# Optimization experiments

Hardware: AMD Instinct MI355X
Metric: run time of the kernel (lower is better)

## Reference

```python
import jax, jax.numpy as jnp
import numpy as np

ROPE_BASE = 10000.0
NUM_HEADS = 16

def _rotate_half(x):
    d = x.shape[-1] // 2
    return jnp.concatenate([-x[..., d:], x[..., :d]], axis=-1)

def setup_inputs() -> dict:
    key = jax.random.key(0)
    ks = jax.random.split(key, 5)
    b, s, d = 1, 2048, 2048
    scale = 1.0 / np.sqrt(d)
    return {
        "hidden_states": jax.random.normal(ks[0], (b, s, d), jnp.float32),
        "wq": jax.random.normal(ks[1], (d, d), jnp.float32) * scale,
        "wk": jax.random.normal(ks[2], (d, d), jnp.float32) * scale,
        "wv": jax.random.normal(ks[3], (d, d), jnp.float32) * scale,
        "wo": jax.random.normal(ks[4], (d, d), jnp.float32) * scale,
        "position_ids": jnp.broadcast_to(jnp.arange(s, dtype=jnp.int32), (b, s)),
    }

def reference(hidden_states, wq, wk, wv, wo, position_ids):
    b, s, d = hidden_states.shape
    h = NUM_HEADS
    dh = d // h
    # q/k/v projections (torch Linear: y = x @ W^T), split heads -> bhsd
    def proj(w):
        return jnp.einsum('bsd,ed->bse', hidden_states, w).reshape(b, s, h, dh).transpose(0, 2, 1, 3)
    q, k, v = proj(wq), proj(wk), proj(wv)
    # rotary embedding (LLaMA style): freqs over half dim, duplicated
    inv_freq = 1.0 / (ROPE_BASE ** (jnp.arange(0, dh, 2, dtype=jnp.float32) / dh))
    t = jnp.arange(s, dtype=jnp.float32)
    freqs = jnp.einsum('s,f->sf', t, inv_freq)              # [s, dh/2]
    emb = jnp.concatenate([freqs, freqs], axis=-1)          # [s, dh]
    cos = jnp.cos(emb)[position_ids][:, None, :, :]         # [b,1,s,dh]
    sin = jnp.sin(emb)[position_ids][:, None, :, :]
    q = q * cos + _rotate_half(q) * sin
    k = k * cos + _rotate_half(k) * sin
    # full (non-causal) scaled dot-product attention, as in the SDPA fast path
    scores = jnp.einsum('bhqd,bhkd->bhqk', q, k) / jnp.sqrt(jnp.float32(dh))
    attn = jax.nn.softmax(scores, axis=-1)
    out = jnp.einsum('bhqk,bhkd->bhqd', attn, v)            # [b,h,s,dh]
    out = out.transpose(0, 2, 1, 3).reshape(b, s, d)
    return jnp.einsum('bsd,ed->bse', out, wo)
```

## Files before the change

kernel.cpp:

```cpp
#include <hip/hip_runtime.h>

typedef unsigned short ushort_t;
typedef unsigned int uint32;
typedef __attribute__((ext_vector_type(8))) short short8;
typedef __attribute__((ext_vector_type(4))) float f32x4;

#define LDS_LOAD16(gptr, lptr)                                                             \
  __builtin_amdgcn_global_load_lds((const __attribute__((address_space(1))) uint32*)(gptr),\
                                   (__attribute__((address_space(3))) uint32*)(lptr),      \
                                   16, 0, 0)

__device__ __forceinline__ ushort_t f2b(float f) {
  uint32 u = __builtin_bit_cast(uint32, f);
  u += 0x7fffu + ((u >> 16) & 1u);
  return (ushort_t)(u >> 16);
}
__device__ __forceinline__ float b2f(ushort_t b) {
  uint32 u = ((uint32)b) << 16;
  return __builtin_bit_cast(float, u);
}
__device__ __forceinline__ int swz4(int row) { return (row ^ (row >> 2)) & 3; }

constexpr size_t E = (size_t)2048 * 2048;

__global__ __launch_bounds__(256) void k_cvt5(const float* __restrict__ a0, const float* __restrict__ a1,
                                              const float* __restrict__ a2, const float* __restrict__ a3,
                                              const float* __restrict__ a4, ushort_t* __restrict__ out) {
  const float* srcs[5] = {a0, a1, a2, a3, a4};
  const float* s = srcs[blockIdx.y];
  size_t i = ((size_t)blockIdx.x * 256 + threadIdx.x) * 4;
  float4 v = *(const float4*)(s + i);
  ushort4 o;
  o.x = f2b(v.x); o.y = f2b(v.y); o.z = f2b(v.z); o.w = f2b(v.w);
  *(ushort4*)(out + (size_t)blockIdx.y * E + i) = o;
}

__global__ __launch_bounds__(256) void k_gemm_qkv(const ushort_t* __restrict__ A,
                                                  const ushort_t* __restrict__ B0,
                                                  const ushort_t* __restrict__ B1,
                                                  const ushort_t* __restrict__ B2,
                                                  ushort_t* __restrict__ Qm,
                                                  ushort_t* __restrict__ Km,
                                                  ushort_t* __restrict__ Vt) {
  __shared__ ushort_t As[128 * 32];
  __shared__ ushort_t Bs[128 * 32];
  const int tid = threadIdx.x;
  const int lane = tid & 63, wave = tid >> 6;
  const int quad = lane >> 4, l16 = lane & 15;
  const int wm = wave >> 1, wn = wave & 1;
  const int z = blockIdx.z;
  const ushort_t* Bp = (z == 0) ? B0 : (z == 1) ? B1 : B2;
  const size_t row0 = (size_t)blockIdx.y * 128, col0 = (size_t)blockIdx.x * 128;
  const int sw = swz4(l16);

  f32x4 zero = {0.f, 0.f, 0.f, 0.f};
  f32x4 acc[4][4];
#pragma unroll
  for (int i = 0; i < 4; ++i)
#pragma unroll
    for (int j = 0; j < 4; ++j) acc[i][j] = zero;

  for (int kt = 0; kt < 64; ++kt) {
#pragma unroll
    for (int j = 0; j < 2; ++j) {
      int c = tid + 256 * j;
      int r = c >> 2, p = c & 3;
      int srcc = (p ^ swz4(r)) * 8;
      LDS_LOAD16(A + (row0 + r) * 2048 + kt * 32 + srcc, &As[c * 8]);
      LDS_LOAD16(Bp + (col0 + r) * 2048 + kt * 32 + srcc, &Bs[c * 8]);
    }
    __syncthreads();
    short8 a[4], b[4];
#pragma unroll
    for (int i = 0; i < 4; ++i) {
      int ra = wm * 64 + i * 16 + l16;
      int rb = wn * 64 + i * 16 + l16;
      a[i] = *(const short8*)&As[(ra * 4 + (quad ^ sw)) * 8];
      b[i] = *(const short8*)&Bs[(rb * 4 + (quad ^ sw)) * 8];
    }
#pragma unroll
    for (int i = 0; i < 4; ++i)
#pragma unroll
      for (int j = 0; j < 4; ++j)
        acc[i][j] = __builtin_amdgcn_mfma_f32_16x16x32_bf16(a[i], b[j], acc[i][j], 0, 0, 0);
    __syncthreads();
  }

  if (z < 2) {
    ushort_t* C = z ? Km : Qm;
#pragma unroll
    for (int i = 0; i < 4; ++i)
#pragma unroll
      for (int j = 0; j < 4; ++j)
#pragma unroll
        for (int r = 0; r < 4; ++r) {
          size_t row = row0 + wm * 64 + i * 16 + quad * 4 + r;
          size_t col = col0 + wn * 64 + j * 16 + l16;
          C[row * 2048 + col] = f2b(acc[i][j][r]);
        }
  } else {
#pragma unroll
    for (int i = 0; i < 4; ++i)
#pragma unroll
      for (int j = 0; j < 4; ++j) {
        size_t col = col0 + wn * 64 + j * 16 + l16;
        size_t rowb = row0 + wm * 64 + i * 16 + quad * 4;
        ushort4 ov;
        ov.x = f2b(acc[i][j][0]); ov.y = f2b(acc[i][j][1]);
        ov.z = f2b(acc[i][j][2]); ov.w = f2b(acc[i][j][3]);
        *(ushort4*)&Vt[col * 2048 + rowb] = ov;
      }
  }
}

__global__ __launch_bounds__(256) void k_rope(ushort_t* __restrict__ Q,
                                              ushort_t* __restrict__ Kk,
                                              const int* __restrict__ pos) {
  int idx = blockIdx.x * 256 + threadIdx.x;
  int f = idx & 63;
  int h = (idx >> 6) & 15;
  int t = idx >> 10;
  float tp = (float)pos[t];
  float ang = tp * expf(-0.14391156831212787f * (float)f);
  float sn, cs;
  sincosf(ang, &sn, &cs);
  size_t base = (size_t)t * 2048 + h * 128 + f;
  float q0 = b2f(Q[base]), q1 = b2f(Q[base + 64]);
  Q[base]      = f2b(q0 * cs - q1 * sn);
  Q[base + 64] = f2b(q1 * cs + q0 * sn);
  float k0 = b2f(Kk[base]), k1 = b2f(Kk[base + 64]);
  Kk[base]      = f2b(k0 * cs - k1 * sn);
  Kk[base + 64] = f2b(k1 * cs + k0 * sn);
}

__global__ __launch_bounds__(256, 2) void k_attn(const ushort_t* __restrict__ Q,
                                                 const ushort_t* __restrict__ Kg,
                                                 const ushort_t* __restrict__ Vt,
                                                 ushort_t* __restrict__ O) {
  __shared__ ushort_t Qs[64 * 128];
  __shared__ float Rbuf[4][16][132];
  __shared__ float Lred[4][4][16];
  const int tid = threadIdx.x;
  const int lane = tid & 63, wave = tid >> 6;
  const int quad = lane >> 4, l16 = lane & 15;
  const int bid = blockIdx.x;
  const int head = ((bid & 7) << 1) + ((bid >> 3) >> 5);
  const int qt = (bid >> 3) & 31;

#pragma unroll
  for (int j = 0; j < 4; ++j) {
    int s = tid + 256 * j;
    int r = s >> 4, p = s & 15;
    LDS_LOAD16(Q + (size_t)(qt * 64 + r) * 2048 + head * 128 + ((p ^ (r & 15)) * 8), &Qs[s * 8]);
  }
  __syncthreads();

  f32x4 zero = {0.f, 0.f, 0.f, 0.f};
  f32x4 oacc[4][8];
#pragma unroll
  for (int qg = 0; qg < 4; ++qg)
#pragma unroll
    for (int ns = 0; ns < 8; ++ns) oacc[qg][ns] = zero;
  float l_acc[4] = {0.f, 0.f, 0.f, 0.f};
  const float scale = 0.08838834764831845f;
  const int srcA = ((quad & 1) << 5) | l16;
  const int srcB = srcA + 16;
  const bool hiq = quad >= 2;

  const ushort_t* Kbase = Kg + (size_t)head * 128;
  const ushort_t* Vbase = Vt + (size_t)head * 128 * 2048;

  for (int it = 0; it < 16; ++it) {
    const int kb = it * 128 + wave * 32;

    short8 kf[2][4];
#pragma unroll
    for (int kg = 0; kg < 2; ++kg)
#pragma unroll
      for (int kk = 0; kk < 4; ++kk)
        kf[kg][kk] = *(const short8*)&Kbase[(size_t)(kb + kg * 16 + l16) * 2048 + kk * 32 + quad * 8];

    uint32 pp[4][2][2];
#pragma unroll
    for (int qg = 0; qg < 4; ++qg) {
      short8 qa[4];
#pragma unroll
      for (int kk = 0; kk < 4; ++kk)
        qa[kk] = *(const short8*)&Qs[((qg * 16 + l16) * 16 + ((kk * 4 + quad) ^ l16)) * 8];
      f32x4 s0 = zero, s1 = zero;
#pragma unroll
      for (int kk = 0; kk < 4; ++kk) {
        s0 = __builtin_amdgcn_mfma_f32_16x16x32_bf16(kf[0][kk], qa[kk], s0, 0, 0, 0);
        s1 = __builtin_amdgcn_mfma_f32_16x16x32_bf16(kf[1][kk], qa[kk], s1, 0, 0, 0);
      }
      float p00 = __expf(s0[0] * scale), p01 = __expf(s0[1] * scale);
      float p02 = __expf(s0[2] * scale), p03 = __expf(s0[3] * scale);
      float p10 = __expf(s1[0] * scale), p11 = __expf(s1[1] * scale);
      float p12 = __expf(s1[2] * scale), p13 = __expf(s1[3] * scale);
      l_acc[qg] += ((p00 + p01) + (p02 + p03)) + ((p10 + p11) + (p12 + p13));
      pp[qg][0][0] = (uint32)f2b(p00) | ((uint32)f2b(p01) << 16);
      pp[qg][0][1] = (uint32)f2b(p02) | ((uint32)f2b(p03) << 16);
      pp[qg][1][0] = (uint32)f2b(p10) | ((uint32)f2b(p11) << 16);
      pp[qg][1][1] = (uint32)f2b(p12) | ((uint32)f2b(p13) << 16);
    }

    short8 pb[4];
#pragma unroll
    for (int qg = 0; qg < 4; ++qg) {
      uint32 a0 = (uint32)__shfl((int)pp[qg][0][0], srcA, 64);
      uint32 b0 = (uint32)__shfl((int)pp[qg][1][0], srcA, 64);
      uint32 a1 = (uint32)__shfl((int)pp[qg][0][1], srcA, 64);
      uint32 b1 = (uint32)__shfl((int)pp[qg][1][1], srcA, 64);
      uint32 a2 = (uint32)__shfl((int)pp[qg][0][0], srcB, 64);
      uint32 b2 = (uint32)__shfl((int)pp[qg][1][0], srcB, 64);
      uint32 a3 = (uint32)__shfl((int)pp[qg][0][1], srcB, 64);
      uint32 b3 = (uint32)__shfl((int)pp[qg][1][1], srcB, 64);
      union { uint32 u[4]; short8 v; } cvt;
      cvt.u[0] = hiq ? b0 : a0;
      cvt.u[1] = hiq ? b1 : a1;
      cvt.u[2] = hiq ? b2 : a2;
      cvt.u[3] = hiq ? b3 : a3;
      pb[qg] = cvt.v;
    }

#pragma unroll
    for (int ns = 0; ns < 8; ++ns) {
      const short8 vf = *(const short8*)&Vbase[(size_t)(ns * 16 + l16) * 2048 + kb + quad * 8];
#pragma unroll
      for (int qg = 0; qg < 4; ++qg)
        oacc[qg][ns] = __builtin_amdgcn_mfma_f32_16x16x32_bf16(vf, pb[qg], oacc[qg][ns], 0, 0, 0);
    }
  }

#pragma unroll
  for (int qg = 0; qg < 4; ++qg) {
    float l = l_acc[qg];
    l += __shfl_xor(l, 16, 64);
    l += __shfl_xor(l, 32, 64);
    l_acc[qg] = l;
  }
  if (quad == 0) {
#pragma unroll
    for (int qg = 0; qg < 4; ++qg) Lred[wave][qg][l16] = l_acc[qg];
  }

  const int tq = tid >> 4;
  const int td = (tid & 15) * 8;
  for (int qg = 0; qg < 4; ++qg) {
    __syncthreads();
#pragma unroll
    for (int ns = 0; ns < 8; ++ns)
      *(f32x4*)&Rbuf[wave][l16][ns * 16 + quad * 4] = oacc[qg][ns];
    __syncthreads();
    float lt = Lred[0][qg][tq] + Lred[1][qg][tq] + Lred[2][qg][tq] + Lred[3][qg][tq];
    float inv = 1.0f / lt;
    f32x4 sA = zero, sB = zero;
#pragma unroll
    for (int w = 0; w < 4; ++w) {
      sA += *(const f32x4*)&Rbuf[w][tq][td];
      sB += *(const f32x4*)&Rbuf[w][tq][td + 4];
    }
    ushort4 o1, o2;
    o1.x = f2b(sA[0] * inv); o1.y = f2b(sA[1] * inv);
    o1.z = f2b(sA[2] * inv); o1.w = f2b(sA[3] * inv);
    o2.x = f2b(sB[0] * inv); o2.y = f2b(sB[1] * inv);
    o2.z = f2b(sB[2] * inv); o2.w = f2b(sB[3] * inv);
    size_t orow = (size_t)(qt * 64 + qg * 16 + tq) * 2048 + head * 128 + td;
    *(ushort4*)&O[orow] = o1;
    *(ushort4*)&O[orow + 4] = o2;
  }
}

__global__ __launch_bounds__(256) void k_gemm_wo(const ushort_t* __restrict__ A,
                                                 const ushort_t* __restrict__ B,
                                                 float* __restrict__ C) {
  __shared__ ushort_t As[128 * 32];
  __shared__ ushort_t Bs[64 * 32];
  const int tid = threadIdx.x;
  const int lane = tid & 63, wave = tid >> 6;
  const int quad = lane >> 4, l16 = lane & 15;
  const int wm = wave >> 1, wn = wave & 1;
  const size_t row0 = (size_t)blockIdx.y * 128, col0 = (size_t)blockIdx.x * 64;
  const int sw = swz4(l16);

  f32x4 zero = {0.f, 0.f, 0.f, 0.f};
  f32x4 acc[4][2];
#pragma unroll
  for (int i = 0; i < 4; ++i)
#pragma unroll
    for (int j = 0; j < 2; ++j) acc[i][j] = zero;

  for (int kt = 0; kt < 64; ++kt) {
#pragma unroll
    for (int j = 0; j < 2; ++j) {
      int c = tid + 256 * j;
      int r = c >> 2, p = c & 3;
      LDS_LOAD16(A + (row0 + r) * 2048 + kt * 32 + (p ^ swz4(r)) * 8, &As[c * 8]);
    }
    {
      int c = tid;
      int r = c >> 2, p = c & 3;
      LDS_LOAD16(B + (col0 + r) * 2048 + kt * 32 + (p ^ swz4(r)) * 8, &Bs[c * 8]);
    }
    __syncthreads();
    short8 a[4], b[2];
#pragma unroll
    for (int i = 0; i < 4; ++i)
      a[i] = *(const short8*)&As[((wm * 64 + i * 16 + l16) * 4 + (quad ^ sw)) * 8];
#pragma unroll
    for (int j = 0; j < 2; ++j)
      b[j] = *(const short8*)&Bs[((wn * 32 + j * 16 + l16) * 4 + (quad ^ sw)) * 8];
#pragma unroll
    for (int i = 0; i < 4; ++i)
#pragma unroll
      for (int j = 0; j < 2; ++j)
        acc[i][j] = __builtin_amdgcn_mfma_f32_16x16x32_bf16(a[i], b[j], acc[i][j], 0, 0, 0);
    __syncthreads();
  }

#pragma unroll
  for (int i = 0; i < 4; ++i)
#pragma unroll
    for (int j = 0; j < 2; ++j)
#pragma unroll
      for (int r = 0; r < 4; ++r) {
        size_t row = row0 + wm * 64 + i * 16 + quad * 4 + r;
        size_t col = col0 + wn * 32 + j * 16 + l16;
        C[row * 2048 + col] = acc[i][j][r];
      }
}

extern "C" void kernel_launch(void* const* d_in, const int* in_sizes, int n_in,
                              void* d_out, int out_size, void* d_ws, size_t ws_size,
                              hipStream_t stream) {
  const float* X  = (const float*)d_in[0];
  const float* wq = (const float*)d_in[1];
  const float* wk = (const float*)d_in[2];
  const float* wv = (const float*)d_in[3];
  const float* wo = (const float*)d_in[4];
  const int*  pos = (const int*)d_in[5];
  float* out = (float*)d_out;

  if (ws_size < 9 * E * sizeof(ushort_t)) return;

  ushort_t* Xb  = (ushort_t*)d_ws;
  ushort_t* Wqb = Xb + E;
  ushort_t* Wkb = Xb + 2 * E;
  ushort_t* Wvb = Xb + 3 * E;
  ushort_t* Wob = Xb + 4 * E;
  ushort_t* Qm  = Xb + 5 * E;
  ushort_t* Km  = Xb + 6 * E;
  ushort_t* Vtm = Xb + 7 * E;
  ushort_t* Om  = Xb + 8 * E;

  dim3 b256(256);
  k_cvt5<<<dim3(4096, 5), b256, 0, stream>>>(X, wq, wk, wv, wo, Xb);
  k_gemm_qkv<<<dim3(16, 16, 3), b256, 0, stream>>>(Xb, Wqb, Wkb, Wvb, Qm, Km, Vtm);
  k_rope<<<8192, b256, 0, stream>>>(Qm, Km, pos);
  k_attn<<<512, b256, 0, stream>>>(Qm, Km, Vtm, Om);
  k_gemm_wo<<<dim3(32, 16), b256, 0, stream>>>(Om, Wob, out);
}
```

Measured before the change: 332.0 us.

## Fuse RoPE and softmax scale into QKV GEMM epilogue, widen K tile to 64

Removes the separate RoPE kernel and applies the rotation, plus the 1/sqrt(dh) scale on Q, inside the QKV GEMM epilogue. Each wave's column assignment is remapped so it holds both halves of a head's rotary pair. Both GEMMs now stage 64-wide K tiles with an 8-way swizzle, halving the loop iterations and barriers. The fusion saves a full read-modify-write pass over Q and K, at the cost of a heavier epilogue and doubled LDS per block, which may lower occupancy.

```diff
diff --git a/kernel.cpp b/kernel.cpp
--- a/kernel.cpp
+++ b/kernel.cpp
@@ -19,7 +19,10 @@
   uint32 u = ((uint32)b) << 16;
   return __builtin_bit_cast(float, u);
 }
-__device__ __forceinline__ int swz4(int row) { return (row ^ (row >> 2)) & 3; }
+__device__ __forceinline__ uint32 pk2(float a, float b) {
+  return (uint32)f2b(a) | ((uint32)f2b(b) << 16);
+}
+__device__ __forceinline__ int swz8(int r) { return (r ^ (r >> 3)) & 7; }
 
 constexpr size_t E = (size_t)2048 * 2048;
 
@@ -41,9 +44,10 @@
                                                   const ushort_t* __restrict__ B2,
                                                   ushort_t* __restrict__ Qm,
                                                   ushort_t* __restrict__ Km,
-                                                  ushort_t* __restrict__ Vt) {
-  __shared__ ushort_t As[128 * 32];
-  __shared__ ushort_t Bs[128 * 32];
+                                                  ushort_t* __restrict__ Vt,
+                                                  const int* __restrict__ pos) {
+  __shared__ ushort_t As[128 * 64];
+  __shared__ ushort_t Bs[128 * 64];
   const int tid = threadIdx.x;
   const int lane = tid & 63, wave = tid >> 6;
   const int quad = lane >> 4, l16 = lane & 15;
@@ -51,7 +55,10 @@
   const int z = blockIdx.z;
   const ushort_t* Bp = (z == 0) ? B0 : (z == 1) ? B1 : B2;
   const size_t row0 = (size_t)blockIdx.y * 128, col0 = (size_t)blockIdx.x * 128;
-  const int sw = swz4(l16);
+
+  int g[4];
+#pragma unroll
+  for (int j = 0; j < 4; ++j) g[j] = (j & 1) + ((j >> 1) << 2) + wn * 2;
 
   f32x4 zero = {0.f, 0.f, 0.f, 0.f};
   f32x4 acc[4][4];
@@ -60,50 +67,69 @@
 #pragma unroll
     for (int j = 0; j < 4; ++j) acc[i][j] = zero;
 
-  for (int kt = 0; kt < 64; ++kt) {
-#pragma unroll
-    for (int j = 0; j < 2; ++j) {
-      int c = tid + 256 * j;
-      int r = c >> 2, p = c & 3;
-      int srcc = (p ^ swz4(r)) * 8;
-      LDS_LOAD16(A + (row0 + r) * 2048 + kt * 32 + srcc, &As[c * 8]);
-      LDS_LOAD16(Bp + (col0 + r) * 2048 + kt * 32 + srcc, &Bs[c * 8]);
-    }
-    __syncthreads();
-    short8 a[4], b[4];
+  for (int kt = 0; kt < 32; ++kt) {
+#pragma unroll
+    for (int j2 = 0; j2 < 4; ++j2) {
+      int c = tid + 256 * j2;
+      int r = c >> 3, p = c & 7;
+      int sc = (p ^ swz8(r)) * 8;
+      LDS_LOAD16(A + (row0 + r) * 2048 + kt * 64 + sc, &As[c * 8]);
+      LDS_LOAD16(Bp + (col0 + r) * 2048 + kt * 64 + sc, &Bs[c * 8]);
+    }
+    __syncthreads();
+    short8 a[4][2], b[4][2];
 #pragma unroll
     for (int i = 0; i < 4; ++i) {
       int ra = wm * 64 + i * 16 + l16;
-      int rb = wn * 64 + i * 16 + l16;
-      a[i] = *(const short8*)&As[(ra * 4 + (quad ^ sw)) * 8];
-      b[i] = *(const short8*)&Bs[(rb * 4 + (quad ^ sw)) * 8];
-    }
-#pragma unroll
-    for (int i = 0; i < 4; ++i)
-#pragma unroll
-      for (int j = 0; j < 4; ++j)
-        acc[i][j] = __builtin_amdgcn_mfma_f32_16x16x32_bf16(a[i], b[j], acc[i][j], 0, 0, 0);
+#pragma unroll
+      for (int kk = 0; kk < 2; ++kk)
+        a[i][kk] = *(const short8*)&As[(ra * 8 + ((kk * 4 + quad) ^ swz8(ra))) * 8];
+    }
+#pragma unroll
+    for (int j = 0; j < 4; ++j) {
+      int rb = g[j] * 16 + l16;
+#pragma unroll
+      for (int kk = 0; kk < 2; ++kk)
+        b[j][kk] = *(const short8*)&Bs[(rb * 8 + ((kk * 4 + quad) ^ swz8(rb))) * 8];
+    }
+#pragma unroll
+    for (int kk = 0; kk < 2; ++kk)
+#pragma unroll
+      for (int i = 0; i < 4; ++i)
+#pragma unroll
+        for (int j = 0; j < 4; ++j)
+          acc[i][j] = __builtin_amdgcn_mfma_f32_16x16x32_bf16(a[i][kk], b[j][kk], acc[i][j], 0, 0, 0);
     __syncthreads();
   }
 
   if (z < 2) {
     ushort_t* C = z ? Km : Qm;
+    const float mul = z ? 1.0f : 0.08838834764831845f;
 #pragma unroll
     for (int i = 0; i < 4; ++i)
 #pragma unroll
-      for (int j = 0; j < 4; ++j)
-#pragma unroll
-        for (int r = 0; r < 4; ++r) {
-          size_t row = row0 + wm * 64 + i * 16 + quad * 4 + r;
-          size_t col = col0 + wn * 64 + j * 16 + l16;
-          C[row * 2048 + col] = f2b(acc[i][j][r]);
+      for (int r = 0; r < 4; ++r) {
+        size_t row = row0 + wm * 64 + i * 16 + quad * 4 + r;
+        float pt = (float)pos[row];
+        size_t rowoff = row * 2048 + col0;
+#pragma unroll
+        for (int j = 0; j < 2; ++j) {
+          int f = g[j] * 16 + l16;
+          float ang = pt * __expf(-0.14391156831212787f * (float)f);
+          float sn, cs;
+          __sincosf(ang, &sn, &cs);
+          cs *= mul; sn *= mul;
+          float q0 = acc[i][j][r], q1 = acc[i][j + 2][r];
+          C[rowoff + f]      = f2b(q0 * cs - q1 * sn);
+          C[rowoff + f + 64] = f2b(q1 * cs + q0 * sn);
         }
+      }
   } else {
 #pragma unroll
     for (int i = 0; i < 4; ++i)
 #pragma unroll
       for (int j = 0; j < 4; ++j) {
-        size_t col = col0 + wn * 64 + j * 16 + l16;
+        size_t col = col0 + g[j] * 16 + l16;
         size_t rowb = row0 + wm * 64 + i * 16 + quad * 4;
         ushort4 ov;
         ov.x = f2b(acc[i][j][0]); ov.y = f2b(acc[i][j][1]);
@@ -111,26 +137,6 @@
         *(ushort4*)&Vt[col * 2048 + rowb] = ov;
       }
   }
-}
-
-__global__ __launch_bounds__(256) void k_rope(ushort_t* __restrict__ Q,
-                                              ushort_t* __restrict__ Kk,
-                                              const int* __restrict__ pos) {
-  int idx = blockIdx.x * 256 + threadIdx.x;
-  int f = idx & 63;
-  int h = (idx >> 6) & 15;
-  int t = idx >> 10;
-  float tp = (float)pos[t];
-  float ang = tp * expf(-0.14391156831212787f * (float)f);
-  float sn, cs;
-  sincosf(ang, &sn, &cs);
-  size_t base = (size_t)t * 2048 + h * 128 + f;
-  float q0 = b2f(Q[base]), q1 = b2f(Q[base + 64]);
-  Q[base]      = f2b(q0 * cs - q1 * sn);
-  Q[base + 64] = f2b(q1 * cs + q0 * sn);
-  float k0 = b2f(Kk[base]), k1 = b2f(Kk[base + 64]);
-  Kk[base]      = f2b(k0 * cs - k1 * sn);
-  Kk[base + 64] = f2b(k1 * cs + k0 * sn);
 }
 
 __global__ __launch_bounds__(256, 2) void k_attn(const ushort_t* __restrict__ Q,
@@ -162,7 +168,6 @@
 #pragma unroll
     for (int ns = 0; ns < 8; ++ns) oacc[qg][ns] = zero;
   float l_acc[4] = {0.f, 0.f, 0.f, 0.f};
-  const float scale = 0.08838834764831845f;
   const int srcA = ((quad & 1) << 5) | l16;
   const int srcB = srcA + 16;
   const bool hiq = quad >= 2;
@@ -193,15 +198,15 @@
         s0 = __builtin_amdgcn_mfma_f32_16x16x32_bf16(kf[0][kk], qa[kk], s0, 0, 0, 0);
         s1 = __builtin_amdgcn_mfma_f32_16x16x32_bf16(kf[1][kk], qa[kk], s1, 0, 0, 0);
       }
-      float p00 = __expf(s0[0] * scale), p01 = __expf(s0[1] * scale);
-      float p02 = __expf(s0[2] * scale), p03 = __expf(s0[3] * scale);
-      float p10 = __expf(s1[0] * scale), p11 = __expf(s1[1] * scale);
-      float p12 = __expf(s1[2] * scale), p13 = __expf(s1[3] * scale);
+      float p00 = __expf(s0[0]), p01 = __expf(s0[1]);
+      float p02 = __expf(s0[2]), p03 = __expf(s0[3]);
+      float p10 = __expf(s1[0]), p11 = __expf(s1[1]);
+      float p12 = __expf(s1[2]), p13 = __expf(s1[3]);
       l_acc[qg] += ((p00 + p01) + (p02 + p03)) + ((p10 + p11) + (p12 + p13));
-      pp[qg][0][0] = (uint32)f2b(p00) | ((uint32)f2b(p01) << 16);
-      pp[qg][0][1] = (uint32)f2b(p02) | ((uint32)f2b(p03) << 16);
-      pp[qg][1][0] = (uint32)f2b(p10) | ((uint32)f2b(p11) << 16);
-      pp[qg][1][1] = (uint32)f2b(p12) | ((uint32)f2b(p13) << 16);
+      pp[qg][0][0] = pk2(p00, p01);
+      pp[qg][0][1] = pk2(p02, p03);
+      pp[qg][1][0] = pk2(p10, p11);
+      pp[qg][1][1] = pk2(p12, p13);
     }
 
     short8 pb[4];
@@ -210,7 +215,7 @@
       uint32 a0 = (uint32)__shfl((int)pp[qg][0][0], srcA, 64);
       uint32 b0 = (uint32)__shfl((int)pp[qg][1][0], srcA, 64);
       uint32 a1 = (uint32)__shfl((int)pp[qg][0][1], srcA, 64);
-      uint32 b1 = (uint32)__shfl((int)pp[qg][1][1], srcA, 64);
+      uint32 b1 = (uint32)__shfl((int)pp[qg][1][1], srcB - 16, 64);
       uint32 a2 = (uint32)__shfl((int)pp[qg][0][0], srcB, 64);
       uint32 b2 = (uint32)__shfl((int)pp[qg][1][0], srcB, 64);
       uint32 a3 = (uint32)__shfl((int)pp[qg][0][1], srcB, 64);
@@ -274,14 +279,13 @@
 __global__ __launch_bounds__(256) void k_gemm_wo(const ushort_t* __restrict__ A,
                                                  const ushort_t* __restrict__ B,
                                                  float* __restrict__ C) {
-  __shared__ ushort_t As[128 * 32];
-  __shared__ ushort_t Bs[64 * 32];
+  __shared__ ushort_t As[128 * 64];
+  __shared__ ushort_t Bs[64 * 64];
   const int tid = threadIdx.x;
   const int lane = tid & 63, wave = tid >> 6;
   const int quad = lane >> 4, l16 = lane & 15;
   const int wm = wave >> 1, wn = wave & 1;
   const size_t row0 = (size_t)blockIdx.y * 128, col0 = (size_t)blockIdx.x * 64;
-  const int sw = swz4(l16);
 
   f32x4 zero = {0.f, 0.f, 0.f, 0.f};
   f32x4 acc[4][2];
@@ -290,31 +294,42 @@
 #pragma unroll
     for (int j = 0; j < 2; ++j) acc[i][j] = zero;
 
-  for (int kt = 0; kt < 64; ++kt) {
+  for (int kt = 0; kt < 32; ++kt) {
+#pragma unroll
+    for (int j2 = 0; j2 < 4; ++j2) {
+      int c = tid + 256 * j2;
+      int r = c >> 3, p = c & 7;
+      LDS_LOAD16(A + (row0 + r) * 2048 + kt * 64 + (p ^ swz8(r)) * 8, &As[c * 8]);
+    }
+#pragma unroll
+    for (int j2 = 0; j2 < 2; ++j2) {
+      int c = tid + 256 * j2;
+      int r = c >> 3, p = c & 7;
+      LDS_LOAD16(B + (col0 + r) * 2048 + kt * 64 + (p ^ swz8(r)) * 8, &Bs[c * 8]);
+    }
+    __syncthreads();
+    short8 a[4][2], b[2][2];
+#pragma unroll
+    for (int i = 0; i < 4; ++i) {
+      int ra = wm * 64 + i * 16 + l16;
+#pragma unroll
+      for (int kk = 0; kk < 2; ++kk)
+        a[i][kk] = *(const short8*)&As[(ra * 8 + ((kk * 4 + quad) ^ swz8(ra))) * 8];
+    }
 #pragma unroll
     for (int j = 0; j < 2; ++j) {
-      int c = tid + 256 * j;
-      int r = c >> 2, p = c & 3;
-      LDS_LOAD16(A + (row0 + r) * 2048 + kt * 32 + (p ^ swz4(r)) * 8, &As[c * 8]);
-    }
-    {
-      int c = tid;
-      int r = c >> 2, p = c & 3;
-      LDS_LOAD16(B + (col0 + r) * 2048 + kt * 32 + (p ^ swz4(r)) * 8, &Bs[c * 8]);
-    }
-    __syncthreads();
-    short8 a[4], b[2];
-#pragma unroll
-    for (int i = 0; i < 4; ++i)
-      a[i] = *(const short8*)&As[((wm * 64 + i * 16 + l16) * 4 + (quad ^ sw)) * 8];
-#pragma unroll
-    for (int j = 0; j < 2; ++j)
-      b[j] = *(const short8*)&Bs[((wn * 32 + j * 16 + l16) * 4 + (quad ^ sw)) * 8];
-#pragma unroll
-    for (int i = 0; i < 4; ++i)
-#pragma unroll
-      for (int j = 0; j < 2; ++j)
-        acc[i][j] = __builtin_amdgcn_mfma_f32_16x16x32_bf16(a[i], b[j], acc[i][j], 0, 0, 0);
+      int rb = wn * 32 + j * 16 + l16;
+#pragma unroll
+      for (int kk = 0; kk < 2; ++kk)
+        b[j][kk] = *(const short8*)&Bs[(rb * 8 + ((kk * 4 + quad) ^ swz8(rb))) * 8];
+    }
+#pragma unroll
+    for (int kk = 0; kk < 2; ++kk)
+#pragma unroll
+      for (int i = 0; i < 4; ++i)
+#pragma unroll
+        for (int j = 0; j < 2; ++j)
+          acc[i][j] = __builtin_amdgcn_mfma_f32_16x16x32_bf16(a[i][kk], b[j][kk], acc[i][j], 0, 0, 0);
     __syncthreads();
   }
 
@@ -355,8 +370,7 @@
 
   dim3 b256(256);
   k_cvt5<<<dim3(4096, 5), b256, 0, stream>>>(X, wq, wk, wv, wo, Xb);
-  k_gemm_qkv<<<dim3(16, 16, 3), b256, 0, stream>>>(Xb, Wqb, Wkb, Wvb, Qm, Km, Vtm);
-  k_rope<<<8192, b256, 0, stream>>>(Qm, Km, pos);
+  k_gemm_qkv<<<dim3(16, 16, 3), b256, 0, stream>>>(Xb, Wqb, Wkb, Wvb, Qm, Km, Vtm, pos);
   k_attn<<<512, b256, 0, stream>>>(Qm, Km, Vtm, Om);
   k_gemm_wo<<<dim3(32, 16), b256, 0, stream>>>(Om, Wob, out);
 }
```

New measurement: 318.0 us. 4.2% less time.
